# Performance work log

Measured on AMD Instinct MI355X. Metric: run time of the kernel, lower is better.

Reference implementation:

```python
import jax, jax.numpy as jnp
import numpy as np

B, T, V, E, H = 1024, 256, 90, 8, 256


def setup_inputs() -> dict:
    key = jax.random.key(0)
    ks = jax.random.split(key, 40)
    rn = lambda k, shape: jax.random.normal(k, shape, dtype=jnp.float32) * 0.05
    inp = {}
    inp["input_seq"] = jax.random.randint(ks[0], (B, T), 0, V, dtype=jnp.int32)
    inp["emb"] = rn(ks[1], (V, E)).at[0].set(0.0)  # padding_idx=0
    i = 2
    for name, din in [("g1", E), ("g2", H), ("l1", E), ("l2", H)]:
        inp[name + "_Wih"] = rn(ks[i], (4 * H, din)); i += 1
        inp[name + "_Whh"] = rn(ks[i], (4 * H, H)); i += 1
        inp[name + "_bih"] = rn(ks[i], (4 * H,)); i += 1
        inp[name + "_bhh"] = rn(ks[i], (4 * H,)); i += 1
    for name in ["p1", "p2"]:
        inp[name + "_W1"] = rn(ks[i], (2 * H, E + 4 * H)); i += 1
        inp[name + "_b1"] = rn(ks[i], (2 * H,)); i += 1
        inp[name + "_W2"] = rn(ks[i], (H, 2 * H)); i += 1
        inp[name + "_b2"] = rn(ks[i], (H,)); i += 1
        inp[name + "_W3"] = rn(ks[i], (2, H)); i += 1
        inp[name + "_b3"] = rn(ks[i], (2,)); i += 1
    inp["gfc_W"] = rn(ks[i], (V, H)); i += 1
    inp["gfc_b"] = rn(ks[i], (V,)); i += 1
    inp["lfc_W"] = rn(ks[i], (V, H)); i += 1
    inp["lfc_b"] = rn(ks[i], (V,))
    return inp


def _cell(x, h, c, Wih, Whh, bih, bhh):
    # PyTorch LSTMCell: gate order i, f, g, o
    g = x @ Wih.T + h @ Whh.T + (bih + bhh)
    i, f, gg, o = jnp.split(g, 4, axis=-1)
    c = jax.nn.sigmoid(f) * c + jax.nn.sigmoid(i) * jnp.tanh(gg)
    return jax.nn.sigmoid(o) * jnp.tanh(c), c


def _mlp(x, W1, b1, W2, b2, W3, b3):
    h = jax.nn.relu(x @ W1.T + b1)
    h = jax.nn.relu(h @ W2.T + b2)
    return h @ W3.T + b3


def _forward(input_seq, emb,
             g1_Wih, g1_Whh, g1_bih, g1_bhh, g2_Wih, g2_Whh, g2_bih, g2_bhh,
             l1_Wih, l1_Whh, l1_bih, l1_bhh, l2_Wih, l2_Whh, l2_bih, l2_bhh,
             p1_W1, p1_b1, p1_W2, p1_b2, p1_W3, p1_b3,
             p2_W1, p2_b1, p2_W2, p2_b2, p2_W3, p2_b3,
             gfc_W, gfc_b, lfc_W, lfc_b):
    Bn = input_seq.shape[0]
    embeds = emb[input_seq]  # [B, T, E]
    z = jnp.zeros((Bn, H), dtype=emb.dtype)

    def step(carry, e):
        gh1, gc1, gh2, gc2, lh1, lc1, lh2, lc2 = carry
        gh1, gc1 = _cell(e, gh1, gc1, g1_Wih, g1_Whh, g1_bih, g1_bhh)
        lh1, lc1 = _cell(e, lh1, lc1, l1_Wih, l1_Whh, l1_bih, l1_bhh)
        p = jax.nn.softmax(_mlp(jnp.concatenate([e, gh1, gc1, lh1, lc1], 1),
                                p1_W1, p1_b1, p1_W2, p1_b2, p1_W3, p1_b3), axis=1)
        # bmm([B,1,2],[B,2,H]) == p0*local + p1*global
        gh1 = p[:, 0:1] * lh1 + p[:, 1:2] * gh1
        gc1 = p[:, 0:1] * lc1 + p[:, 1:2] * gc1
        gh2, gc2 = _cell(gh1, gh2, gc2, g2_Wih, g2_Whh, g2_bih, g2_bhh)
        lh2, lc2 = _cell(lh1, lh2, lc2, l2_Wih, l2_Whh, l2_bih, l2_bhh)
        p = jax.nn.softmax(_mlp(jnp.concatenate([e, gh2, gc2, lh2, lc2], 1),
                                p2_W1, p2_b1, p2_W2, p2_b2, p2_W3, p2_b3), axis=1)
        gh2 = p[:, 0:1] * lh2 + p[:, 1:2] * gh2
        gc2 = p[:, 0:1] * lc2 + p[:, 1:2] * gc2
        return (gh1, gc1, gh2, gc2, lh1, lc1, lh2, lc2), gh2

    _, hs = jax.lax.scan(step, (z, z, z, z, z, z, z, z), jnp.swapaxes(embeds, 0, 1))
    hs = jnp.swapaxes(hs, 0, 1)  # [B, T, H]
    out = 0.5 * (hs @ gfc_W.T + gfc_b) + 0.5 * (hs @ lfc_W.T + lfc_b)
    return jnp.swapaxes(out, 1, 2)  # [B, V, T]


def reference(input_seq, emb,
              g1_Wih, g1_Whh, g1_bih, g1_bhh, g2_Wih, g2_Whh, g2_bih, g2_bhh,
              l1_Wih, l1_Whh, l1_bih, l1_bhh, l2_Wih, l2_Whh, l2_bih, l2_bhh,
              p1_W1, p1_b1, p1_W2, p1_b2, p1_W3, p1_b3,
              p2_W1, p2_b1, p2_W2, p2_b2, p2_W3, p2_b3,
              gfc_W, gfc_b, lfc_W, lfc_b):
    return _forward(input_seq, emb,
                    g1_Wih, g1_Whh, g1_bih, g1_bhh, g2_Wih, g2_Whh, g2_bih, g2_bhh,
                    l1_Wih, l1_Whh, l1_bih, l1_bhh, l2_Wih, l2_Whh, l2_bih, l2_bhh,
                    p1_W1, p1_b1, p1_W2, p1_b2, p1_W3, p1_b3,
                    p2_W1, p2_b1, p2_W2, p2_b2, p2_W3, p2_b3,
                    gfc_W, gfc_b, lfc_W, lfc_b)
```

## Files before the change

kernel.cpp:

```cpp
#include <hip/hip_runtime.h>

#define B_ 1024
#define T_ 256
#define V_ 90
#define H_ 256
#define NTHR 512
#define NBLK 256
#define S_ ((size_t)B_*H_)

typedef unsigned short u16;
typedef __attribute__((ext_vector_type(8))) _Float16 f16x8;
typedef __attribute__((ext_vector_type(4))) _Float16 f16x4;
typedef __attribute__((ext_vector_type(4))) float f32x4;

constexpr size_t OFF_GH1C  = 0;
constexpr size_t OFF_GC1C  = OFF_GH1C + S_;
constexpr size_t OFF_GH1P  = OFF_GC1C + S_;
constexpr size_t OFF_GC1P  = OFF_GH1P + S_;
constexpr size_t OFF_LH1   = OFF_GC1P + S_;
constexpr size_t OFF_LC1   = OFF_LH1 + 2*S_;
constexpr size_t OFF_GH2C  = OFF_LC1 + 2*S_;
constexpr size_t OFF_GC2C  = OFF_GH2C + S_;
constexpr size_t OFF_GH2P  = OFF_GC2C + S_;
constexpr size_t OFF_GC2P  = OFF_GH2P + S_;
constexpr size_t OFF_LH2   = OFF_GC2P + S_;
constexpr size_t OFF_LC2   = OFF_LH2 + 2*S_;
constexpr size_t OFF_M1A   = OFF_LC2 + 2*S_;
constexpr size_t OFF_M1B   = OFF_M1A + (size_t)B_*512;
constexpr size_t OFF_M2A   = OFF_M1B + (size_t)B_*512;
constexpr size_t OFF_M2B   = OFF_M2A + (size_t)B_*512;
constexpr size_t OFF_EX    = OFF_M2B + (size_t)B_*512;
constexpr size_t OFF_WG1PK = OFF_EX + 2*B_*8;
constexpr size_t OFF_WE1   = OFF_WG1PK + 256*2048/2;
constexpr size_t OFF_BG1   = OFF_WE1 + 8*2048;
constexpr size_t OFF_WL2PK = OFF_BG1 + 2048;
constexpr size_t OFF_BL2   = OFF_WL2PK + 512*1024/2;
constexpr size_t OFF_WG2PK = OFF_BL2 + 1024;
constexpr size_t OFF_BG2   = OFF_WG2PK + 512*1024/2;
constexpr size_t OFF_WP1PK = OFF_BG2 + 1024;
constexpr size_t OFF_WEP1  = OFF_WP1PK + 1024*512/2;
constexpr size_t OFF_WP2PK = OFF_WEP1 + 8*512;
constexpr size_t OFF_WEP2  = OFF_WP2PK + 1024*512/2;
constexpr size_t OFF_WB1   = OFF_WEP2 + 8*512;
constexpr size_t OFF_WB2   = OFF_WB1 + 512*256;
constexpr size_t OFF_WOUT  = OFF_WB2 + 512*256;
constexpr size_t OFF_BOUT  = OFF_WOUT + 256*96;
constexpr size_t OFF_BAR   = OFF_BOUT + 128;
constexpr size_t WS_FLOATS = OFF_BAR + 8192;

struct InP {
  const int*   seq;
  const float* emb;
  const float *g1_Wih,*g1_Whh,*g1_bih,*g1_bhh;
  const float *g2_Wih,*g2_Whh,*g2_bih,*g2_bhh;
  const float *l1_Wih,*l1_Whh,*l1_bih,*l1_bhh;
  const float *l2_Wih,*l2_Whh,*l2_bih,*l2_bhh;
  const float *p1_W1,*p1_b1,*p1_W2,*p1_b2,*p1_W3,*p1_b3;
  const float *p2_W1,*p2_b1,*p2_W2,*p2_b2,*p2_W3,*p2_b3;
  const float *gfc_W,*gfc_b,*lfc_W,*lfc_b;
};

__device__ __forceinline__ float sig_(float x)  { return 1.f/(1.f+__expf(-x)); }
__device__ __forceinline__ float tanh_(float x) { return 1.f - 2.f/(__expf(2.f*x)+1.f); }
__device__ __forceinline__ u16 f2h(float v) {
  _Float16 h = (_Float16)v; return __builtin_bit_cast(unsigned short, h);
}

__device__ __forceinline__ unsigned ld_flag(const unsigned* p) {
  unsigned v;
  asm volatile("global_load_dword %0, %1, off sc1\n\ts_waitcnt vmcnt(0)"
               : "=v"(v) : "v"(p) : "memory");
  return v;
}
__device__ __forceinline__ void st_flag(unsigned* p, unsigned v) {
  asm volatile("global_store_dword %0, %1, off sc1\n\ts_waitcnt vmcnt(0)"
               :: "v"(p), "v"(v) : "memory");
}

__device__ __forceinline__ void gbar_x(unsigned* arr, int slot, unsigned ep)
{
  __syncthreads();
  if (threadIdx.x == 0) st_flag(&arr[slot*16], ep);
  if (threadIdx.x < 32) {
    int cap = 0;
    for (;;) {
      unsigned v = ld_flag(&arr[threadIdx.x*16]);
      if (v >= ep) break;
      __builtin_amdgcn_s_sleep(1);
      if (++cap > 200000) break;
    }
  }
  __syncthreads();
  asm volatile("buffer_inv sc0" ::: "memory");
}

template<int NCH, int NSEG, bool HASE, class FE>
__device__ __forceinline__ void mm_h(
    u16* sAB, float* sWe, float* sE,
    const float* s0, const float* s1_,
    const u16* Wpk, int wstep,
    const float* WeP, int ldwe, const float* ex,
    int r0, int ct0, FE fe)
{
  constexpr int BUFU = 6144;
  const int tid = threadIdx.x;
  const int lane = tid & 63;
  const int wr = (tid >> 6) & 3, wc = tid >> 8;
  const int ar = tid >> 3, ak = (tid & 7) << 2;

  __syncthreads();

  if (HASE) {
    for (int i = tid; i < 8*128; i += NTHR)
      sWe[i] = WeP[(i >> 7) * ldwe + ct0 + (i & 127)];
    sE[tid] = ex[((r0 + ar) << 3) + (tid & 7)];
  }

  f32x4 acc[4] = {{0,0,0,0},{0,0,0,0},{0,0,0,0},{0,0,0,0}};

  auto lda = [&](int c) -> float4 {
    int k0 = c * 32;
    const float* S = (NSEG == 1) ? s0 : ((k0 < 256) ? s0 : s1_);
    return *(const float4*)&S[(size_t)(r0 + ar) * H_ + (k0 & 255) + ak];
  };
  auto ldw = [&](int c) -> float4 {
    const float* p = (const float*)(Wpk + (size_t)c * wstep) + tid * 4;
    return *(const float4*)p;
  };
  auto storec = [&](int pb, const float4& pa, const float4& pw) {
    float vv[4] = {pa.x, pa.y, pa.z, pa.w};
    f16x4 hv;
#pragma unroll
    for (int j = 0; j < 4; ++j) hv[j] = (_Float16)vv[j];
    u16* base = sAB + pb*BUFU;
    const int aoff = (ar >> 4)*512 + ((ar & 15) + ((ak >> 3) << 4))*8 + (ak & 7);
    *(f16x4*)(base + aoff) = hv;
    *(float4*)((float*)(base + 2048) + tid*4) = pw;
  };
  auto compute = [&](int pb) {
    u16* base = sAB + pb*BUFU;
    f16x8 a = *(const f16x8*)(base + wr*512 + lane*8);
    const u16* Bp = base + 2048 + (wc*4)*512 + lane*8;
#pragma unroll
    for (int t = 0; t < 4; ++t) {
      f16x8 b = *(const f16x8*)(Bp + t*512);
      acc[t] = __builtin_amdgcn_mfma_f32_16x16x32_f16(a, b, acc[t], 0, 0, 0);
    }
  };

  float4 pa0, pa1, pw0, pw1;
  pa0 = lda(0); pw0 = ldw(0);
  pa1 = lda(1); pw1 = ldw(1);
  storec(0, pa0, pw0);
  __syncthreads();
  for (int c = 0; c < NCH; c += 2) {
    if (c + 2 < NCH) { pa0 = lda(c+2); pw0 = ldw(c+2); }
    compute(0);
    storec(1, pa1, pw1);
    __syncthreads();
    if (c + 3 < NCH) { pa1 = lda(c+3); pw1 = ldw(c+3); }
    compute(1);
    if (c + 2 < NCH) storec(0, pa0, pw0);
    __syncthreads();
  }

  if (HASE) {
#pragma unroll
    for (int t = 0; t < 4; ++t) {
      const int colL = wc*64 + t*16 + (lane & 15);
      float w[8];
#pragma unroll
      for (int j = 0; j < 8; ++j) w[j] = sWe[j*128 + colL];
#pragma unroll
      for (int m = 0; m < 4; ++m) {
        const int rr = wr*16 + ((lane >> 4) << 2) + m;
        float s = 0.f;
#pragma unroll
        for (int j = 0; j < 8; ++j) s = __builtin_fmaf(sE[rr*8 + j], w[j], s);
        acc[t][m] += s;
      }
    }
  }
  fe(wr, wc, lane, acc);
}

struct GateEpiM {
  const float* cin; float* ho; float* co; const float* bias_pk;
  int r0; int ct0; int hb0;
  __device__ void operator()(int wr, int wc, int lane, f32x4 (&acc)[4]) const {
    const int h = hb0 + wc*16 + (lane & 15);
    const int rbase = r0 + wr*16 + ((lane >> 4) << 2);
    float b[4];
#pragma unroll
    for (int t = 0; t < 4; ++t) b[t] = bias_pk[ct0 + wc*64 + t*16 + (lane & 15)];
#pragma unroll
    for (int m = 0; m < 4; ++m) {
      const size_t ix = (size_t)(rbase + m)*H_ + h;
      float gi = sig_(acc[0][m] + b[0]);
      float gf = sig_(acc[1][m] + b[1]);
      float gg = tanh_(acc[2][m] + b[2]);
      float go = sig_(acc[3][m] + b[3]);
      float cn = gf*cin[ix] + gi*gg;
      ho[ix] = go*tanh_(cn); co[ix] = cn;
    }
  }
};

struct MlpEpiM {
  float* dst; int r0; int ct0;
  __device__ void operator()(int wr, int wc, int lane, f32x4 (&acc)[4]) const {
    const int rbase = r0 + wr*16 + ((lane >> 4) << 2);
    const int c0 = ct0 + wc*64 + (lane & 15);
#pragma unroll
    for (int t = 0; t < 4; ++t)
#pragma unroll
      for (int m = 0; m < 4; ++m)
        dst[(size_t)(rbase + m)*512 + c0 + t*16] = acc[t][m];
  }
};

__device__ __forceinline__ void stage_F2(
    int rowbase,
    const float* mlpA, const float* mlpB, const float* b1,
    const float* WB, const float* b2,
    const float* W3, const float* b3,
    const float* lh, const float* lc,
    const float* ghp, const float* gcp,
    float* ghc, float* gcc)
{
  const int w = threadIdx.x >> 6, lane = threadIdx.x & 63;
  const int r0 = rowbase + w*2;
  const float* aA0 = mlpA + (size_t)r0*512; const float* aB0 = mlpB + (size_t)r0*512;
  const float* aA1 = aA0 + 512;             const float* aB1 = aB0 + 512;
  float m0[4] = {0.f,0.f,0.f,0.f}, m1[4] = {0.f,0.f,0.f,0.f};
  for (int k0 = 0; k0 < 512; k0 += 4) {
    float4 xa = *(const float4*)&aA0[k0];
    float4 xb = *(const float4*)&aB0[k0];
    float4 ya = *(const float4*)&aA1[k0];
    float4 yb = *(const float4*)&aB1[k0];
    float4 bb = *(const float4*)&b1[k0];
    float xv0[4] = { fmaxf(xa.x+xb.x+bb.x,0.f), fmaxf(xa.y+xb.y+bb.y,0.f),
                     fmaxf(xa.z+xb.z+bb.z,0.f), fmaxf(xa.w+xb.w+bb.w,0.f) };
    float xv1[4] = { fmaxf(ya.x+yb.x+bb.x,0.f), fmaxf(ya.y+yb.y+bb.y,0.f),
                     fmaxf(ya.z+yb.z+bb.z,0.f), fmaxf(ya.w+yb.w+bb.w,0.f) };
#pragma unroll
    for (int j = 0; j < 4; ++j) {
      float4 wv = *(const float4*)&WB[(size_t)(k0+j)*256 + lane*4];
      m0[0] = __builtin_fmaf(xv0[j], wv.x, m0[0]);
      m0[1] = __builtin_fmaf(xv0[j], wv.y, m0[1]);
      m0[2] = __builtin_fmaf(xv0[j], wv.z, m0[2]);
      m0[3] = __builtin_fmaf(xv0[j], wv.w, m0[3]);
      m1[0] = __builtin_fmaf(xv1[j], wv.x, m1[0]);
      m1[1] = __builtin_fmaf(xv1[j], wv.y, m1[1]);
      m1[2] = __builtin_fmaf(xv1[j], wv.z, m1[2]);
      m1[3] = __builtin_fmaf(xv1[j], wv.w, m1[3]);
    }
  }
  float4 b = *(const float4*)&b2[lane*4];
  float bb2[4] = {b.x,b.y,b.z,b.w};
#pragma unroll
  for (int j = 0; j < 4; ++j) {
    m0[j] = fmaxf(m0[j]+bb2[j], 0.f);
    m1[j] = fmaxf(m1[j]+bb2[j], 0.f);
  }
  float4 w30 = *(const float4*)&W3[lane*4];
  float4 w31 = *(const float4*)&W3[256 + lane*4];
  float w0v[4] = {w30.x,w30.y,w30.z,w30.w};
  float w1v[4] = {w31.x,w31.y,w31.z,w31.w};
  float d00=0.f, d01=0.f, d10=0.f, d11=0.f;
#pragma unroll
  for (int j = 0; j < 4; ++j) {
    d00 = __builtin_fmaf(m0[j], w0v[j], d00);
    d01 = __builtin_fmaf(m0[j], w1v[j], d01);
    d10 = __builtin_fmaf(m1[j], w0v[j], d10);
    d11 = __builtin_fmaf(m1[j], w1v[j], d11);
  }
#pragma unroll
  for (int off = 32; off; off >>= 1) {
    d00 += __shfl_xor(d00, off, 64); d01 += __shfl_xor(d01, off, 64);
    d10 += __shfl_xor(d10, off, 64); d11 += __shfl_xor(d11, off, 64);
  }
  d00 += b3[0]; d01 += b3[1]; d10 += b3[0]; d11 += b3[1];
  float mxa = fmaxf(d00, d01), mxb = fmaxf(d10, d11);
  float e00 = __expf(d00-mxa), e01 = __expf(d01-mxa);
  float e10 = __expf(d10-mxb), e11 = __expf(d11-mxb);
  float ia = 1.f/(e00+e01), ib = 1.f/(e10+e11);
  float p0a = e00*ia, p1a = e01*ia;
  float p0b = e10*ib, p1b = e11*ib;
#pragma unroll
  for (int rr = 0; rr < 2; ++rr) {
    const float p0 = rr ? p0b : p0a, p1 = rr ? p1b : p1a;
    const size_t ix = (size_t)(r0+rr)*H_ + lane*4;
    float4 lv = *(const float4*)&lh[ix];
    float4 gv = *(const float4*)&ghp[ix];
    float4 o;
    o.x = p0*lv.x + p1*gv.x; o.y = p0*lv.y + p1*gv.y;
    o.z = p0*lv.z + p1*gv.z; o.w = p0*lv.w + p1*gv.w;
    *(float4*)&ghc[ix] = o;
    lv = *(const float4*)&lc[ix];
    gv = *(const float4*)&gcp[ix];
    o.x = p0*lv.x + p1*gv.x; o.y = p0*lv.y + p1*gv.y;
    o.z = p0*lv.z + p1*gv.z; o.w = p0*lv.w + p1*gv.w;
    *(float4*)&gcc[ix] = o;
  }
}

__device__ __forceinline__ void stage_OUT2(
    const float* gh2c, const float* WOUT, const float* BOUT,
    float* out, int rbase, int tt)
{
  const int w = threadIdx.x >> 6, lane = threadIdx.x & 63;
  const bool two = lane < (V_ - 64);
#pragma unroll
  for (int rr = 0; rr < 2; ++rr) {
    const int r = rbase + w*2 + rr;
    const float* arow = gh2c + (size_t)r * H_;
    float acc0 = 0.f, acc1 = 0.f;
    for (int k0 = 0; k0 < 256; k0 += 4) {
      float4 a4 = *(const float4*)&arow[k0];
      float av[4] = {a4.x, a4.y, a4.z, a4.w};
#pragma unroll
      for (int j = 0; j < 4; ++j) {
        const float* wr_ = &WOUT[(size_t)(k0+j)*96];
        acc0 = __builtin_fmaf(av[j], wr_[lane], acc0);
        if (two) acc1 = __builtin_fmaf(av[j], wr_[64+lane], acc1);
      }
    }
    out[((size_t)r*V_ + lane)*T_ + tt] = acc0 + BOUT[lane];
    if (two) out[((size_t)r*V_ + 64 + lane)*T_ + tt] = acc1 + BOUT[64+lane];
  }
}

__global__ void k_setup(InP in, float* __restrict__ ws)
{
  const size_t nthr = (size_t)gridDim.x * blockDim.x;
  const size_t t0 = (size_t)blockIdx.x * blockDim.x + threadIdx.x;

  for (size_t i = t0; i < 16*S_; i += nthr) ws[i] = 0.f;
  for (size_t i = t0; i < 8192; i += nthr) ((unsigned*)(ws + OFF_BAR))[i] = 0u;

  for (size_t i = t0; i < (size_t)B_*8; i += nthr) {
    int r = (int)(i >> 3), j = (int)(i & 7);
    ws[OFF_EX + i] = in.emb[(size_t)in.seq[(size_t)r*T_]*8 + j];
  }

  {
    u16* dst = (u16*)(ws + OFF_WG1PK);
    for (size_t i = t0; i < (size_t)8*128*512; i += nthr) {
      int e = (int)(i & 7), lane = (int)((i >> 3) & 63);
      int tile = (int)((i >> 9) & 127), ck = (int)(i >> 16);
      int p = tile*16 + (lane & 15);
      int k = ck*32 + ((lane >> 4) << 3) + e;
      int cell = p >> 10, q = p & 1023;
      int h = ((q >> 6) << 4) + (q & 15), g = (q >> 4) & 3, R = g*256 + h;
      float w = (cell ? in.l1_Whh : in.g1_Whh)[(size_t)R*256 + k];
      dst[((size_t)(ck*128 + tile))*512 + lane*8 + e] = f2h(w);
    }
  }
  for (size_t i = t0; i < (size_t)8*2048; i += nthr) {
    int j = (int)(i >> 11), p = (int)(i & 2047);
    int cell = p >> 10, q = p & 1023;
    int h = ((q >> 6) << 4) + (q & 15), g = (q >> 4) & 3, R = g*256 + h;
    ws[OFF_WE1 + (size_t)j*2048 + p] = (cell ? in.l1_Wih : in.g1_Wih)[(size_t)R*8 + j];
  }
  for (size_t i = t0; i < 2048; i += nthr) {
    int p = (int)i, cell = p >> 10, q = p & 1023;
    int h = ((q >> 6) << 4) + (q & 15), g = (q >> 4) & 3, R = g*256 + h;
    ws[OFF_BG1 + i] = cell ? (in.l1_bih[R] + in.l1_bhh[R]) : (in.g1_bih[R] + in.g1_bhh[R]);
  }

  for (int which = 0; which < 2; ++which) {
    u16* dst = (u16*)(ws + (which ? OFF_WG2PK : OFF_WL2PK));
    const float* Wih = which ? in.g2_Wih : in.l2_Wih;
    const float* Whh = which ? in.g2_Whh : in.l2_Whh;
    for (size_t i = t0; i < (size_t)16*64*512; i += nthr) {
      int e = (int)(i & 7), lane = (int)((i >> 3) & 63);
      int tile = (int)((i >> 9) & 63), ck = (int)(i >> 15);
      int p = tile*16 + (lane & 15);
      int k = ck*32 + ((lane >> 4) << 3) + e;
      int h = ((p >> 6) << 4) + (p & 15), g = (p >> 4) & 3, R = g*256 + h;
      float w = (k < 256) ? Wih[(size_t)R*256 + k] : Whh[(size_t)R*256 + (k-256)];
      dst[((size_t)(ck*64 + tile))*512 + lane*8 + e] = f2h(w);
    }
  }
  for (size_t i = t0; i < 2*1024; i += nthr) {
    int which = (int)(i >> 10), p = (int)(i & 1023);
    int h = ((p >> 6) << 4) + (p & 15), g = (p >> 4) & 3, R = g*256 + h;
    float v = which ? (in.g2_bih[R] + in.g2_bhh[R]) : (in.l2_bih[R] + in.l2_bhh[R]);
    ws[(which ? OFF_BG2 : OFF_BL2) + p] = v;
  }

  for (int which = 0; which < 2; ++which) {
    u16* dst = (u16*)(ws + (which ? OFF_WP2PK : OFF_WP1PK));
    const float* W = which ? in.p2_W1 : in.p1_W1;
    for (size_t i = t0; i < (size_t)32*32*512; i += nthr) {
      int e = (int)(i & 7), lane = (int)((i >> 3) & 63);
      int tile = (int)((i >> 9) & 31), ck = (int)(i >> 14);
      int p = tile*16 + (lane & 15);
      int k = ck*32 + ((lane >> 4) << 3) + e;
      dst[((size_t)(ck*32 + tile))*512 + lane*8 + e] = f2h(W[(size_t)p*1032 + 8 + k]);
    }
  }
  for (size_t i = t0; i < (size_t)2*8*512; i += nthr) {
    int which = (int)(i / (8*512));
    int idx = (int)(i - (size_t)which*8*512);
    int j = idx >> 9, p = idx & 511;
    const float* W = which ? in.p2_W1 : in.p1_W1;
    ws[(which ? OFF_WEP2 : OFF_WEP1) + (size_t)j*512 + p] = W[(size_t)p*1032 + j];
  }

  for (size_t i = t0; i < (size_t)2*512*256; i += nthr) {
    int which = (int)(i / (512*256));
    int idx = (int)(i - (size_t)which*512*256);
    int k = idx >> 8, n = idx & 255;
    const float* W = which ? in.p2_W2 : in.p1_W2;
    ws[(which ? OFF_WB2 : OFF_WB1) + idx] = W[(size_t)n*512 + k];
  }
  for (size_t i = t0; i < (size_t)256*96; i += nthr) {
    int k = (int)(i / 96), c = (int)(i - (size_t)k*96);
    float v = 0.f;
    if (c < V_) v = 0.5f*(in.gfc_W[(size_t)c*256 + k] + in.lfc_W[(size_t)c*256 + k]);
    ws[OFF_WOUT + i] = v;
  }
  for (size_t i = t0; i < 96; i += nthr)
    ws[OFF_BOUT + i] = (i < V_) ? 0.5f*(in.gfc_b[i] + in.lfc_b[i]) : 0.f;
}

__global__ __launch_bounds__(NTHR) void k_main(InP in, float* ws, float* __restrict__ out)
{
  __shared__ __attribute__((aligned(16))) u16   sAB[2*6144];
  __shared__ __attribute__((aligned(16))) float sWe[8*128];
  __shared__ __attribute__((aligned(16))) float sE[512];

  float* GH1C = ws + OFF_GH1C;  float* GC1C = ws + OFF_GC1C;
  float* GH1P = ws + OFF_GH1P;  float* GC1P = ws + OFF_GC1P;
  float* LH1  = ws + OFF_LH1;   float* LC1  = ws + OFF_LC1;
  float* GH2C = ws + OFF_GH2C;  float* GC2C = ws + OFF_GC2C;
  float* GH2P = ws + OFF_GH2P;  float* GC2P = ws + OFF_GC2P;
  float* LH2  = ws + OFF_LH2;   float* LC2  = ws + OFF_LC2;
  float* M1A  = ws + OFF_M1A;   float* M1B  = ws + OFF_M1B;
  float* M2A  = ws + OFF_M2A;   float* M2B  = ws + OFF_M2B;
  float* EXB  = ws + OFF_EX;
  const u16* WG1PK = (const u16*)(ws + OFF_WG1PK);
  const u16* WL2PK = (const u16*)(ws + OFF_WL2PK);
  const u16* WG2PK = (const u16*)(ws + OFF_WG2PK);
  const u16* WP1PK = (const u16*)(ws + OFF_WP1PK);
  const u16* WP2PK = (const u16*)(ws + OFF_WP2PK);
  const float* WE1  = ws + OFF_WE1;  const float* BG1P = ws + OFF_BG1;
  const float* BL2P = ws + OFF_BL2;  const float* BG2P = ws + OFF_BG2;
  const float* WEP1 = ws + OFF_WEP1; const float* WEP2 = ws + OFF_WEP2;
  const float* WB1  = ws + OFF_WB1;  const float* WB2  = ws + OFF_WB2;
  const float* WOUT = ws + OFF_WOUT; const float* BOUT = ws + OFF_BOUT;

  unsigned xcc;
  asm volatile("s_getreg_b32 %0, hwreg(HW_REG_XCC_ID)" : "=s"(xcc));
  xcc &= 7u;
  unsigned* barx = ((unsigned*)(ws + OFF_BAR)) + xcc*1024;
  unsigned* arr  = barx;
  unsigned* reg  = barx + 544;
  __shared__ unsigned s_slot;
  if (threadIdx.x == 0)
    s_slot = __hip_atomic_fetch_add(reg, 1u, __ATOMIC_RELAXED, __HIP_MEMORY_SCOPE_AGENT);
  __syncthreads();
  const int slot  = (int)(s_slot & 31u);
  const int rows0 = (int)xcc * 128;
  unsigned ep = 0;

  for (int n = 0; n <= T_; ++n) {
    const int sel = n & 1;
    const float* ex  = EXB + sel*(B_*8);
    const float* exm = EXB + (sel^1)*(B_*8);
    float* lh1o = LH1 + sel*S_;   float* lh1n = LH1 + (sel^1)*S_;
    float* lc1o = LC1 + sel*S_;   float* lc1n = LC1 + (sel^1)*S_;
    float* lh2o = LH2 + sel*S_;   float* lh2n = LH2 + (sel^1)*S_;
    float* lc2o = LC2 + sel*S_;   float* lc2n = LC2 + (sel^1)*S_;

    if (slot < 16) {
      if (n < T_) {
        const int rt = slot & 1, cq = slot >> 1;
        const int r0 = rows0 + rt*64;
        const int cell = cq >> 2;
        const float* hin = cell ? lh1o : GH1C;
#pragma unroll
        for (int half = 0; half < 2; ++half) {
          const int ct0 = cq*256 + half*128;
          GateEpiM epi{ cell ? lc1o : GC1C,
                        cell ? lh1n : GH1P,
                        cell ? lc1n : GC1P,
                        BG1P, r0, ct0, ((ct0 & 1023) >> 6) << 4 };
          mm_h<8,1,true>(sAB, sWe, sE, hin, nullptr,
                         WG1PK + (size_t)(ct0 >> 4)*512, 128*512,
                         WE1, 2048, ex, r0, ct0, epi);
        }
      }
    } else if (n >= 1) {
      const int s2 = slot - 16;
      const int rt = s2 & 1, ct = s2 >> 1;
      const int r0 = rows0 + rt*64, ct0 = ct*128;
      GateEpiM epi{ GC2C, GH2P, GC2P, BG2P, r0, ct0, (ct0 >> 6) << 4 };
      mm_h<16,2,false>(sAB, sWe, sE, GH1C, GH2C,
                       WG2PK + (size_t)(ct0 >> 4)*512, 64*512,
                       nullptr, 0, nullptr, r0, ct0, epi);
    }
    gbar_x(arr, slot, ++ep);

    if (slot < 16) {
      if (n < T_) {
        const int rt = slot & 1, q = slot >> 1;
        const int ct = q & 3, kh = q >> 2;
        const int r0 = rows0 + rt*64, ct0 = ct*128;
        if (kh == 0) {
          MlpEpiM epi{ M1A, r0, ct0 };
          mm_h<16,2,false>(sAB, sWe, sE, GH1P, GC1P,
                           WP1PK + (size_t)(ct0 >> 4)*512, 32*512,
                           nullptr, 0, nullptr, r0, ct0, epi);
        } else {
          MlpEpiM epi{ M1B, r0, ct0 };
          mm_h<16,2,true>(sAB, sWe, sE, lh1n, lc1n,
                          WP1PK + (size_t)16*(32*512) + (size_t)(ct0 >> 4)*512, 32*512,
                          WEP1, 512, ex, r0, ct0, epi);
        }
      }
    } else if (n >= 1) {
      const int s2 = slot - 16;
      const int rt = s2 & 1, q = s2 >> 1;
      const int ct = q & 3, kh = q >> 2;
      const int r0 = rows0 + rt*64, ct0 = ct*128;
      if (kh == 0) {
        MlpEpiM epi{ M2A, r0, ct0 };
        mm_h<16,2,false>(sAB, sWe, sE, GH2P, GC2P,
                         WP2PK + (size_t)(ct0 >> 4)*512, 32*512,
                         nullptr, 0, nullptr, r0, ct0, epi);
      } else {
        MlpEpiM epi{ M2B, r0, ct0 };
        mm_h<16,2,true>(sAB, sWe, sE, lh2o, lc2o,
                        WP2PK + (size_t)16*(32*512) + (size_t)(ct0 >> 4)*512, 32*512,
                        WEP2, 512, exm, r0, ct0, epi);
      }
    }
    gbar_x(arr, slot, ++ep);

    if (slot < 16) {
      if (n < T_) {
        const int rt = slot & 1, ct = slot >> 1;
        const int r0 = rows0 + rt*64, ct0 = ct*128;
        GateEpiM epi{ lc2o, lh2n, lc2n, BL2P, r0, ct0, (ct0 >> 6) << 4 };
        mm_h<16,2,false>(sAB, sWe, sE, lh1n, lh2o,
                         WL2PK + (size_t)(ct0 >> 4)*512, 64*512,
                         nullptr, 0, nullptr, r0, ct0, epi);
      }
    } else if (slot < 24) {
      if (n < T_) {
        const int rb = rows0 + (slot-16)*16;
        stage_F2(rb, M1A, M1B, in.p1_b1, WB1, in.p1_b2, in.p1_W3, in.p1_b3,
                 lh1n, lc1n, GH1P, GC1P, GH1C, GC1C);
        if (n + 1 < T_ && threadIdx.x < 128) {
          const int r = rb + (threadIdx.x >> 3), j = threadIdx.x & 7;
          EXB[(sel^1)*(B_*8) + r*8 + j] =
              in.emb[(size_t)in.seq[(size_t)r*T_ + n + 1]*8 + j];
        }
      }
    } else {
      if (n >= 1) {
        const int rb = rows0 + (slot-24)*16;
        stage_F2(rb, M2A, M2B, in.p2_b1, WB2, in.p2_b2, in.p2_W3, in.p2_b3,
                 lh2o, lc2o, GH2P, GC2P, GH2C, GC2C);
        __syncthreads();
        stage_OUT2(GH2C, WOUT, BOUT, out, rb, n-1);
      }
    }
    gbar_x(arr, slot, ++ep);
  }
}

extern "C" void kernel_launch(void* const* d_in, const int* in_sizes, int n_in,
                              void* d_out, int out_size, void* d_ws, size_t ws_size,
                              hipStream_t stream)
{
  if (ws_size < WS_FLOATS * sizeof(float)) return;

  InP in;
  in.seq    = (const int*)  d_in[0];
  in.emb    = (const float*)d_in[1];
  in.g1_Wih = (const float*)d_in[2];  in.g1_Whh = (const float*)d_in[3];
  in.g1_bih = (const float*)d_in[4];  in.g1_bhh = (const float*)d_in[5];
  in.g2_Wih = (const float*)d_in[6];  in.g2_Whh = (const float*)d_in[7];
  in.g2_bih = (const float*)d_in[8];  in.g2_bhh = (const float*)d_in[9];
  in.l1_Wih = (const float*)d_in[10]; in.l1_Whh = (const float*)d_in[11];
  in.l1_bih = (const float*)d_in[12]; in.l1_bhh = (const float*)d_in[13];
  in.l2_Wih = (const float*)d_in[14]; in.l2_Whh = (const float*)d_in[15];
  in.l2_bih = (const float*)d_in[16]; in.l2_bhh = (const float*)d_in[17];
  in.p1_W1  = (const float*)d_in[18]; in.p1_b1  = (const float*)d_in[19];
  in.p1_W2  = (const float*)d_in[20]; in.p1_b2  = (const float*)d_in[21];
  in.p1_W3  = (const float*)d_in[22]; in.p1_b3  = (const float*)d_in[23];
  in.p2_W1  = (const float*)d_in[24]; in.p2_b1  = (const float*)d_in[25];
  in.p2_W2  = (const float*)d_in[26]; in.p2_b2  = (const float*)d_in[27];
  in.p2_W3  = (const float*)d_in[28]; in.p2_b3  = (const float*)d_in[29];
  in.gfc_W  = (const float*)d_in[30]; in.gfc_b  = (const float*)d_in[31];
  in.lfc_W  = (const float*)d_in[32]; in.lfc_b  = (const float*)d_in[33];

  float* ws  = (float*)d_ws;
  float* out = (float*)d_out;

  k_setup<<<512, 256, 0, stream>>>(in, ws);
  k_main <<<NBLK, NTHR, 53248, stream>>>(in, ws, out);
}
```

Baseline: 63.86 ms.

## Load MFMA operands directly from global into registers, dropping LDS staging

Replaces the LDS double-buffered GEMM tile routine with a register-only version. Each lane loads its A fragment (converted to fp16) and its B fragments straight from global memory, prefetching up to four K-chunks ahead, so the per-chunk __syncthreads calls and LDS round-trips go away. The embedding-term weights and inputs are now read from global memory instead of shared memory. A volatile shared array is kept to pin LDS allocation, presumably to hold occupancy at one block per CU. The trade-off is higher register pressure and redundant global/L2 reads: each B tile is fetched by every row-wave instead of once per block.

```diff
diff --git a/kernel.cpp b/kernel.cpp
--- a/kernel.cpp
+++ b/kernel.cpp
@@ -10,7 +10,6 @@
 
 typedef unsigned short u16;
 typedef __attribute__((ext_vector_type(8))) _Float16 f16x8;
-typedef __attribute__((ext_vector_type(4))) _Float16 f16x4;
 typedef __attribute__((ext_vector_type(4))) float f32x4;
 
 constexpr size_t OFF_GH1C  = 0;
@@ -95,88 +94,66 @@
 }
 
 template<int NCH, int NSEG, bool HASE, class FE>
-__device__ __forceinline__ void mm_h(
-    u16* sAB, float* sWe, float* sE,
+__device__ __forceinline__ void mm_reg(
     const float* s0, const float* s1_,
-    const u16* Wpk, int wstep,
+    const u16* __restrict__ Wpk, int tiles,
     const float* WeP, int ldwe, const float* ex,
     int r0, int ct0, FE fe)
 {
-  constexpr int BUFU = 6144;
-  const int tid = threadIdx.x;
+  const int tid  = threadIdx.x;
   const int lane = tid & 63;
   const int wr = (tid >> 6) & 3, wc = tid >> 8;
-  const int ar = tid >> 3, ak = (tid & 7) << 2;
-
-  __syncthreads();
+  const int row = r0 + wr*16 + (lane & 15);
+  const int kq  = (lane >> 4) << 3;
+
+  f32x4 acc[4] = {{0,0,0,0},{0,0,0,0},{0,0,0,0},{0,0,0,0}};
+
+  constexpr int D = (NCH < 4) ? NCH : 4;
+  float4 alo[D], ahi[D];
+  f16x8  bfr[D][4];
+
+  auto ldA = [&](int c, float4& lo, float4& hi) {
+    const int k0 = c * 32;
+    const float* S = (NSEG == 1) ? s0 : ((k0 < 256) ? s0 : s1_);
+    const float* p = &S[(size_t)row*H_ + (k0 & 255) + kq];
+    lo = *(const float4*)p; hi = *(const float4*)(p + 4);
+  };
+  auto ldB = [&](int c, f16x8* b) {
+    const u16* base = Wpk + ((size_t)c*tiles + wc*4)*512 + lane*8;
+#pragma unroll
+    for (int t = 0; t < 4; ++t) b[t] = *(const f16x8*)(base + (size_t)t*512);
+  };
+  auto comp = [&](const float4& lo, const float4& hi, const f16x8* b) {
+    float av[8] = {lo.x,lo.y,lo.z,lo.w,hi.x,hi.y,hi.z,hi.w};
+    f16x8 a;
+#pragma unroll
+    for (int j = 0; j < 8; ++j) a[j] = (_Float16)av[j];
+#pragma unroll
+    for (int t = 0; t < 4; ++t)
+      acc[t] = __builtin_amdgcn_mfma_f32_16x16x32_f16(a, b[t], acc[t], 0, 0, 0);
+  };
+
+#pragma unroll
+  for (int c = 0; c < D; ++c) { ldA(c, alo[c], ahi[c]); ldB(c, bfr[c]); }
+#pragma unroll
+  for (int c = 0; c < NCH; ++c) {
+    comp(alo[c % D], ahi[c % D], bfr[c % D]);
+    if (c + D < NCH) { ldA(c + D, alo[c % D], ahi[c % D]); ldB(c + D, bfr[c % D]); }
+  }
 
   if (HASE) {
-    for (int i = tid; i < 8*128; i += NTHR)
-      sWe[i] = WeP[(i >> 7) * ldwe + ct0 + (i & 127)];
-    sE[tid] = ex[((r0 + ar) << 3) + (tid & 7)];
-  }
-
-  f32x4 acc[4] = {{0,0,0,0},{0,0,0,0},{0,0,0,0},{0,0,0,0}};
-
-  auto lda = [&](int c) -> float4 {
-    int k0 = c * 32;
-    const float* S = (NSEG == 1) ? s0 : ((k0 < 256) ? s0 : s1_);
-    return *(const float4*)&S[(size_t)(r0 + ar) * H_ + (k0 & 255) + ak];
-  };
-  auto ldw = [&](int c) -> float4 {
-    const float* p = (const float*)(Wpk + (size_t)c * wstep) + tid * 4;
-    return *(const float4*)p;
-  };
-  auto storec = [&](int pb, const float4& pa, const float4& pw) {
-    float vv[4] = {pa.x, pa.y, pa.z, pa.w};
-    f16x4 hv;
-#pragma unroll
-    for (int j = 0; j < 4; ++j) hv[j] = (_Float16)vv[j];
-    u16* base = sAB + pb*BUFU;
-    const int aoff = (ar >> 4)*512 + ((ar & 15) + ((ak >> 3) << 4))*8 + (ak & 7);
-    *(f16x4*)(base + aoff) = hv;
-    *(float4*)((float*)(base + 2048) + tid*4) = pw;
-  };
-  auto compute = [&](int pb) {
-    u16* base = sAB + pb*BUFU;
-    f16x8 a = *(const f16x8*)(base + wr*512 + lane*8);
-    const u16* Bp = base + 2048 + (wc*4)*512 + lane*8;
 #pragma unroll
     for (int t = 0; t < 4; ++t) {
-      f16x8 b = *(const f16x8*)(Bp + t*512);
-      acc[t] = __builtin_amdgcn_mfma_f32_16x16x32_f16(a, b, acc[t], 0, 0, 0);
-    }
-  };
-
-  float4 pa0, pa1, pw0, pw1;
-  pa0 = lda(0); pw0 = ldw(0);
-  pa1 = lda(1); pw1 = ldw(1);
-  storec(0, pa0, pw0);
-  __syncthreads();
-  for (int c = 0; c < NCH; c += 2) {
-    if (c + 2 < NCH) { pa0 = lda(c+2); pw0 = ldw(c+2); }
-    compute(0);
-    storec(1, pa1, pw1);
-    __syncthreads();
-    if (c + 3 < NCH) { pa1 = lda(c+3); pw1 = ldw(c+3); }
-    compute(1);
-    if (c + 2 < NCH) storec(0, pa0, pw0);
-    __syncthreads();
-  }
-
-  if (HASE) {
-#pragma unroll
-    for (int t = 0; t < 4; ++t) {
-      const int colL = wc*64 + t*16 + (lane & 15);
+      const int colL = ct0 + wc*64 + t*16 + (lane & 15);
       float w[8];
 #pragma unroll
-      for (int j = 0; j < 8; ++j) w[j] = sWe[j*128 + colL];
+      for (int j = 0; j < 8; ++j) w[j] = WeP[j*ldwe + colL];
 #pragma unroll
       for (int m = 0; m < 4; ++m) {
-        const int rr = wr*16 + ((lane >> 4) << 2) + m;
+        const int rr = r0 + wr*16 + ((lane >> 4) << 2) + m;
         float s = 0.f;
 #pragma unroll
-        for (int j = 0; j < 8; ++j) s = __builtin_fmaf(sE[rr*8 + j], w[j], s);
+        for (int j = 0; j < 8; ++j) s = __builtin_fmaf(ex[rr*8 + j], w[j], s);
         acc[t][m] += s;
       }
     }
@@ -428,9 +405,8 @@
 
 __global__ __launch_bounds__(NTHR) void k_main(InP in, float* ws, float* __restrict__ out)
 {
-  __shared__ __attribute__((aligned(16))) u16   sAB[2*6144];
-  __shared__ __attribute__((aligned(16))) float sWe[8*128];
-  __shared__ __attribute__((aligned(16))) float sE[512];
+  __shared__ __attribute__((aligned(16))) volatile float s_pin[7680];
+  __shared__ unsigned s_slot;
 
   float* GH1C = ws + OFF_GH1C;  float* GC1C = ws + OFF_GC1C;
   float* GH1P = ws + OFF_GH1P;  float* GC1P = ws + OFF_GC1P;
@@ -458,9 +434,10 @@
   unsigned* barx = ((unsigned*)(ws + OFF_BAR)) + xcc*1024;
   unsigned* arr  = barx;
   unsigned* reg  = barx + 544;
-  __shared__ unsigned s_slot;
-  if (threadIdx.x == 0)
+  if (threadIdx.x == 0) {
     s_slot = __hip_atomic_fetch_add(reg, 1u, __ATOMIC_RELAXED, __HIP_MEMORY_SCOPE_AGENT);
+    s_pin[0] = (float)s_slot;
+  }
   __syncthreads();
   const int slot  = (int)(s_slot & 31u);
   const int rows0 = (int)xcc * 128;
@@ -488,9 +465,9 @@
                         cell ? lh1n : GH1P,
                         cell ? lc1n : GC1P,
                         BG1P, r0, ct0, ((ct0 & 1023) >> 6) << 4 };
-          mm_h<8,1,true>(sAB, sWe, sE, hin, nullptr,
-                         WG1PK + (size_t)(ct0 >> 4)*512, 128*512,
-                         WE1, 2048, ex, r0, ct0, epi);
+          mm_reg<8,1,true>(hin, nullptr,
+                           WG1PK + (size_t)(ct0 >> 4)*512, 128,
+                           WE1, 2048, ex, r0, ct0, epi);
         }
       }
     } else if (n >= 1) {
@@ -498,9 +475,9 @@
       const int rt = s2 & 1, ct = s2 >> 1;
       const int r0 = rows0 + rt*64, ct0 = ct*128;
       GateEpiM epi{ GC2C, GH2P, GC2P, BG2P, r0, ct0, (ct0 >> 6) << 4 };
-      mm_h<16,2,false>(sAB, sWe, sE, GH1C, GH2C,
-                       WG2PK + (size_t)(ct0 >> 4)*512, 64*512,
-                       nullptr, 0, nullptr, r0, ct0, epi);
+      mm_reg<16,2,false>(GH1C, GH2C,
+                         WG2PK + (size_t)(ct0 >> 4)*512, 64,
+                         nullptr, 0, nullptr, r0, ct0, epi);
     }
     gbar_x(arr, slot, ++ep);
 
@@ -511,14 +488,14 @@
         const int r0 = rows0 + rt*64, ct0 = ct*128;
         if (kh == 0) {
           MlpEpiM epi{ M1A, r0, ct0 };
-          mm_h<16,2,false>(sAB, sWe, sE, GH1P, GC1P,
-                           WP1PK + (size_t)(ct0 >> 4)*512, 32*512,
-                           nullptr, 0, nullptr, r0, ct0, epi);
+          mm_reg<16,2,false>(GH1P, GC1P,
+                             WP1PK + (size_t)(ct0 >> 4)*512, 32,
+                             nullptr, 0, nullptr, r0, ct0, epi);
         } else {
           MlpEpiM epi{ M1B, r0, ct0 };
-          mm_h<16,2,true>(sAB, sWe, sE, lh1n, lc1n,
-                          WP1PK + (size_t)16*(32*512) + (size_t)(ct0 >> 4)*512, 32*512,
-                          WEP1, 512, ex, r0, ct0, epi);
+          mm_reg<16,2,true>(lh1n, lc1n,
+                            WP1PK + (size_t)16*(32*512) + (size_t)(ct0 >> 4)*512, 32,
+                            WEP1, 512, ex, r0, ct0, epi);
         }
       }
     } else if (n >= 1) {
@@ -528,14 +505,14 @@
       const int r0 = rows0 + rt*64, ct0 = ct*128;
       if (kh == 0) {
         MlpEpiM epi{ M2A, r0, ct0 };
-        mm_h<16,2,false>(sAB, sWe, sE, GH2P, GC2P,
-                         WP2PK + (size_t)(ct0 >> 4)*512, 32*512,
-                         nullptr, 0, nullptr, r0, ct0, epi);
+        mm_reg<16,2,false>(GH2P, GC2P,
+                           WP2PK + (size_t)(ct0 >> 4)*512, 32,
+                           nullptr, 0, nullptr, r0, ct0, epi);
       } else {
         MlpEpiM epi{ M2B, r0, ct0 };
-        mm_h<16,2,true>(sAB, sWe, sE, lh2o, lc2o,
-                        WP2PK + (size_t)16*(32*512) + (size_t)(ct0 >> 4)*512, 32*512,
-                        WEP2, 512, exm, r0, ct0, epi);
+        mm_reg<16,2,true>(lh2o, lc2o,
+                          WP2PK + (size_t)16*(32*512) + (size_t)(ct0 >> 4)*512, 32,
+                          WEP2, 512, exm, r0, ct0, epi);
       }
     }
     gbar_x(arr, slot, ++ep);
@@ -545,9 +522,9 @@
         const int rt = slot & 1, ct = slot >> 1;
         const int r0 = rows0 + rt*64, ct0 = ct*128;
         GateEpiM epi{ lc2o, lh2n, lc2n, BL2P, r0, ct0, (ct0 >> 6) << 4 };
-        mm_h<16,2,false>(sAB, sWe, sE, lh1n, lh2o,
-                         WL2PK + (size_t)(ct0 >> 4)*512, 64*512,
-                         nullptr, 0, nullptr, r0, ct0, epi);
+        mm_reg<16,2,false>(lh1n, lh2o,
+                           WL2PK + (size_t)(ct0 >> 4)*512, 64,
+                           nullptr, 0, nullptr, r0, ct0, epi);
       }
     } else if (slot < 24) {
       if (n < T_) {
```

Result: slower. 82.05 ms (+28.5%).
